# Kernel tuning notes

Measured on AMD Instinct MI355X. Metric: run time of the kernel, lower is better.

The kernel has to match this reference:

```python
import jax, jax.numpy as jnp
import numpy as np

N = 16000
E = 512000
HID = 128
OUT = 64
BN_EPS = 1e-5


def setup_inputs() -> dict:
    key = jax.random.key(0)
    ks = jax.random.split(key, 8)
    x = jax.random.normal(ks[0], (N, HID), dtype=jnp.float32)
    src = jax.random.randint(ks[1], (E,), 0, N, dtype=jnp.int32)
    dst = jax.random.randint(ks[2], (E,), 0, N, dtype=jnp.int32)
    s = 1.0 / np.sqrt(HID)
    fc_w = jax.random.uniform(ks[3], (OUT, HID), jnp.float32, -s, s)
    fc_b = jnp.zeros((OUT,), jnp.float32)
    w1 = jax.random.uniform(ks[4], (HID, HID), jnp.float32, -s, s)
    b1 = jnp.zeros((HID,), jnp.float32)
    w2 = jax.random.uniform(ks[5], (OUT, HID), jnp.float32, -s, s)
    b2 = jnp.zeros((OUT,), jnp.float32)
    epsilon = jnp.full((N,), 0.5, jnp.float32)
    gamma = jnp.ones((OUT,), jnp.float32)
    beta = jnp.zeros((OUT,), jnp.float32)
    return {"x": x, "src": src, "dst": dst, "fc_w": fc_w, "fc_b": fc_b,
            "w1": w1, "b1": b1, "w2": w2, "b2": b2,
            "epsilon": epsilon, "gamma": gamma, "beta": beta}


def _agg(feat, src, dst, n):
    # DGL update_all(copy_src, sum): gather source features, scatter-sum to dst.
    return jax.ops.segment_sum(feat[src], dst, num_segments=n)


def reference(x, src, dst, fc_w, fc_b, w1, b1, w2, b2, epsilon, gamma, beta):
    n = x.shape[0]
    # skip-path linear projection
    h1 = x @ fc_w.T + fc_b                       # [N, OUT]
    # GraphConv layer 1: aggregate then linear, then ReLU
    h2 = jax.nn.relu(_agg(x, src, dst, n) @ w1.T + b1)   # [N, HID]
    # GraphConv layer 2
    h2 = _agg(h2, src, dst, n) @ w2.T + b2       # [N, OUT]
    # per-node epsilon blend
    eps = epsilon[:, None]
    h = (1.0 - eps) * h1 + eps * h2              # [N, OUT]
    # averaged gram matrices
    ret = (h @ h.T + x @ x.T) * 0.5              # [N, N]
    # BatchNorm1d (training mode: biased batch stats)
    mean = jnp.mean(h, axis=0)
    var = jnp.mean(jnp.square(h - mean), axis=0)
    hn = (h - mean) * jax.lax.rsqrt(var + BN_EPS) * gamma + beta
    return ret, hn
```

## Files before the change

kernel.cpp:

```cpp
#include <hip/hip_runtime.h>
#include <hip/hip_bf16.h>

typedef __bf16 bf16x8 __attribute__((ext_vector_type(8)));
typedef float  f32x4  __attribute__((ext_vector_type(4)));
typedef unsigned short u16x8 __attribute__((ext_vector_type(8)));

#define HID 128
#define OUT 64
#define BN_EPS 1e-5f

__device__ __forceinline__ float bf2f(unsigned short u) {
  union { unsigned int i; float f; } c; c.i = ((unsigned)u) << 16; return c.f;
}

__global__ __launch_bounds__(256) void xconv_k(
    const float* __restrict__ x, unsigned short* __restrict__ xbf,
    int* __restrict__ cnt, int n)
{
  int gid = blockIdx.x * blockDim.x + threadIdx.x;
  if (gid < n) cnt[gid] = 0;
  int stride = gridDim.x * blockDim.x;
  int total = n * 32;
  for (int idx = gid; idx < total; idx += stride) {
    f32x4 v = ((const f32x4*)x)[idx];
    ushort4 o;
    __bf16 b0 = (__bf16)v[0], b1 = (__bf16)v[1], b2 = (__bf16)v[2], b3 = (__bf16)v[3];
    o.x = *(unsigned short*)&b0; o.y = *(unsigned short*)&b1;
    o.z = *(unsigned short*)&b2; o.w = *(unsigned short*)&b3;
    ((ushort4*)xbf)[idx] = o;
  }
}

__global__ __launch_bounds__(256) void hist_k(
    const int* __restrict__ dst, int* __restrict__ cnt, int e)
{
  int stride = gridDim.x * blockDim.x;
  for (int i = blockIdx.x * blockDim.x + threadIdx.x; i < e; i += stride)
    atomicAdd(&cnt[dst[i]], 1);
}

__global__ __launch_bounds__(256) void scan_k(
    const int* __restrict__ cnt, int* __restrict__ offsets,
    int* __restrict__ cursor, float* __restrict__ stats, int n)
{
  int t = threadIdx.x;
  if (t < 128) stats[t] = 0.f;
  __shared__ int part[256];
  int chunk = (n + 255) / 256;
  int base = t * chunk;
  int s = 0;
  for (int i = 0; i < chunk; ++i) {
    int idx = base + i;
    if (idx < n) s += cnt[idx];
  }
  part[t] = s;
  __syncthreads();
  for (int off = 1; off < 256; off <<= 1) {
    int v = 0;
    if (t >= off) v = part[t - off];
    __syncthreads();
    if (t >= off) part[t] += v;
    __syncthreads();
  }
  int run = (t == 0) ? 0 : part[t - 1];
  for (int i = 0; i < chunk; ++i) {
    int idx = base + i;
    if (idx < n) {
      offsets[idx] = run;
      cursor[idx]  = run;
      run += cnt[idx];
    }
  }
  if (t == 255) offsets[n] = run;
}

__global__ __launch_bounds__(256) void place_k(
    const int* __restrict__ src, const int* __restrict__ dst,
    int* __restrict__ cursor, int* __restrict__ sorted_src, int e)
{
  int stride = gridDim.x * blockDim.x;
  for (int i = blockIdx.x * blockDim.x + threadIdx.x; i < e; i += stride) {
    int pos = atomicAdd(&cursor[dst[i]], 1);
    sorted_src[pos] = src[i];
  }
}

__global__ __launch_bounds__(256) void aggx_k(
    const unsigned short* __restrict__ xbf, const int* __restrict__ sorted_src,
    const int* __restrict__ offsets, float* __restrict__ agg, int n)
{
  int wave = (blockIdx.x * 256 + threadIdx.x) >> 6;
  int lane = threadIdx.x & 63;
  if (wave >= n) return;
  int qtr = lane >> 4;
  int l16 = lane & 15;
  int beg = offsets[wave], end = offsets[wave + 1];
  float a0[8] = {}, a1[8] = {};
  int i = beg + qtr;
  for (; i + 4 < end; i += 8) {
    int s0 = sorted_src[i];
    int s1 = sorted_src[i + 4];
    u16x8 v0 = *(const u16x8*)(xbf + (size_t)s0 * HID + l16 * 8);
    u16x8 v1 = *(const u16x8*)(xbf + (size_t)s1 * HID + l16 * 8);
    #pragma unroll
    for (int j = 0; j < 8; ++j) { a0[j] += bf2f(v0[j]); a1[j] += bf2f(v1[j]); }
  }
  if (i < end) {
    int s0 = sorted_src[i];
    u16x8 v0 = *(const u16x8*)(xbf + (size_t)s0 * HID + l16 * 8);
    #pragma unroll
    for (int j = 0; j < 8; ++j) a0[j] += bf2f(v0[j]);
  }
  #pragma unroll
  for (int j = 0; j < 8; ++j) a0[j] += a1[j];
  #pragma unroll
  for (int j = 0; j < 8; ++j) a0[j] += __shfl_xor(a0[j], 16, 64);
  #pragma unroll
  for (int j = 0; j < 8; ++j) a0[j] += __shfl_xor(a0[j], 32, 64);
  if (qtr == 0) {
    f32x4 lo = {a0[0], a0[1], a0[2], a0[3]};
    f32x4 hi = {a0[4], a0[5], a0[6], a0[7]};
    *(f32x4*)(agg + (size_t)wave * HID + l16 * 8)     = lo;
    *(f32x4*)(agg + (size_t)wave * HID + l16 * 8 + 4) = hi;
  }
}

__global__ __launch_bounds__(256) void agg2y_k(
    const unsigned short* __restrict__ y2, const int* __restrict__ sorted_src,
    const int* __restrict__ offsets, float* __restrict__ aggy, int n)
{
  int wave = (blockIdx.x * 256 + threadIdx.x) >> 6;
  int lane = threadIdx.x & 63;
  if (wave >= n) return;
  int qtr = lane >> 4;
  int l16 = lane & 15;
  int beg = offsets[wave], end = offsets[wave + 1];
  f32x4 a0 = {0.f, 0.f, 0.f, 0.f}, a1 = {0.f, 0.f, 0.f, 0.f};
  int i = beg + qtr;
  for (; i + 4 < end; i += 8) {
    int s0 = sorted_src[i];
    int s1 = sorted_src[i + 4];
    ushort4 v0 = *(const ushort4*)(y2 + (size_t)s0 * OUT + l16 * 4);
    ushort4 v1 = *(const ushort4*)(y2 + (size_t)s1 * OUT + l16 * 4);
    a0[0] += bf2f(v0.x); a0[1] += bf2f(v0.y); a0[2] += bf2f(v0.z); a0[3] += bf2f(v0.w);
    a1[0] += bf2f(v1.x); a1[1] += bf2f(v1.y); a1[2] += bf2f(v1.z); a1[3] += bf2f(v1.w);
  }
  if (i < end) {
    int s0 = sorted_src[i];
    ushort4 v0 = *(const ushort4*)(y2 + (size_t)s0 * OUT + l16 * 4);
    a0[0] += bf2f(v0.x); a0[1] += bf2f(v0.y); a0[2] += bf2f(v0.z); a0[3] += bf2f(v0.w);
  }
  a0 += a1;
  f32x4 other;
  #pragma unroll
  for (int j = 0; j < 4; ++j) other[j] = __shfl_xor(a0[j], 16, 64);
  a0 += other;
  #pragma unroll
  for (int j = 0; j < 4; ++j) other[j] = __shfl_xor(a0[j], 32, 64);
  a0 += other;
  if (qtr == 0)
    *(f32x4*)(aggy + (size_t)wave * OUT + l16 * 4) = a0;
}

__global__ __launch_bounds__(256) void mlp_fused_k(
    const float* __restrict__ agg, const float* __restrict__ w1,
    const float* __restrict__ b1, const float* __restrict__ w2,
    unsigned short* __restrict__ y2, int n)
{
  __shared__ float aggs[16][132];
  __shared__ float h2s[16][132];
  int t = threadIdx.x;
  int rbase = blockIdx.x * 16;

  for (int idx = t; idx < 16 * 32; idx += 256) {
    int r = idx >> 5, c = idx & 31;
    ((f32x4*)&aggs[r][0])[c] = ((const f32x4*)(agg + (size_t)(rbase + r) * HID))[c];
  }
  __syncthreads();

  {
    int j = t & 127, rh = t >> 7;
    const f32x4* w1r = (const f32x4*)(w1 + (size_t)j * HID);
    float acc[8];
    float bj = b1[j];
    #pragma unroll
    for (int p = 0; p < 8; ++p) acc[p] = bj;
    for (int k = 0; k < 32; ++k) {
      f32x4 w = w1r[k];
      #pragma unroll
      for (int p = 0; p < 8; ++p) {
        f32x4 a = ((const f32x4*)&aggs[rh * 8 + p][0])[k];
        acc[p] += w[0] * a[0] + w[1] * a[1] + w[2] * a[2] + w[3] * a[3];
      }
    }
    #pragma unroll
    for (int p = 0; p < 8; ++p) h2s[rh * 8 + p][j] = fmaxf(acc[p], 0.f);
  }
  __syncthreads();

  {
    int o = t & 63, rq = t >> 6;
    const f32x4* w2r = (const f32x4*)(w2 + (size_t)o * HID);
    float acc[4] = {0.f, 0.f, 0.f, 0.f};
    for (int k = 0; k < 32; ++k) {
      f32x4 w = w2r[k];
      #pragma unroll
      for (int p = 0; p < 4; ++p) {
        f32x4 a = ((const f32x4*)&h2s[rq + p * 4][0])[k];
        acc[p] += w[0] * a[0] + w[1] * a[1] + w[2] * a[2] + w[3] * a[3];
      }
    }
    #pragma unroll
    for (int p = 0; p < 4; ++p) {
      __bf16 b = (__bf16)acc[p];
      y2[(size_t)(rbase + rq + p * 4) * OUT + o] = *(unsigned short*)&b;
    }
  }
}

__global__ __launch_bounds__(256) void combine_k(
    const float* __restrict__ x, const float* __restrict__ aggy,
    const float* __restrict__ fcw, const float* __restrict__ fcb,
    const float* __restrict__ b2,
    const float* __restrict__ eps, float* __restrict__ h,
    unsigned short* __restrict__ hbf, float* __restrict__ stats, int n)
{
  __shared__ float xs[32][132];
  __shared__ float ls[256], lss[256];
  int t = threadIdx.x;
  int rbase = blockIdx.x * 32;

  for (int idx = t; idx < 32 * 32; idx += 256) {
    int r = idx >> 5, c = idx & 31;
    ((f32x4*)&xs[r][0])[c] = ((const f32x4*)(x + (size_t)(rbase + r) * HID))[c];
  }
  __syncthreads();

  int o = t & 63, rq = t >> 6;
  const f32x4* fwr = (const f32x4*)(fcw + (size_t)o * HID);
  float fb = fcb[o], bb = b2[o];
  float acc[8];
  #pragma unroll
  for (int p = 0; p < 8; ++p) acc[p] = fb;
  for (int k = 0; k < 32; ++k) {
    f32x4 w = fwr[k];
    #pragma unroll
    for (int p = 0; p < 8; ++p) {
      f32x4 a = ((const f32x4*)&xs[rq + p * 4][0])[k];
      acc[p] += w[0] * a[0] + w[1] * a[1] + w[2] * a[2] + w[3] * a[3];
    }
  }
  float s = 0.f, ss = 0.f;
  #pragma unroll
  for (int p = 0; p < 8; ++p) {
    int row = rbase + rq + p * 4;
    float a2 = aggy[(size_t)row * OUT + o] + bb;
    float ev = eps[row];
    float hv = (1.f - ev) * acc[p] + ev * a2;
    h[(size_t)row * OUT + o] = hv;
    __bf16 hb = (__bf16)hv;
    hbf[(size_t)row * OUT + o] = *(unsigned short*)&hb;
    s += hv; ss += hv * hv;
  }
  ls[t] = s; lss[t] = ss;
  __syncthreads();
  if (t < 64) {
    s  = ls[t]  + ls[t + 64]  + ls[t + 128]  + ls[t + 192];
    ss = lss[t] + lss[t + 64] + lss[t + 128] + lss[t + 192];
    atomicAdd(&stats[t], s);
    atomicAdd(&stats[64 + t], ss);
  }
}

__global__ __launch_bounds__(256) void hn_k(
    const float* __restrict__ h, const float* __restrict__ stats,
    const float* __restrict__ gamma, const float* __restrict__ beta,
    float* __restrict__ outp, int n)
{
  int stride = gridDim.x * blockDim.x;
  int total  = n * OUT;
  float inv_n = 1.f / (float)n;
  for (int idx = blockIdx.x * blockDim.x + threadIdx.x; idx < total; idx += stride) {
    int col = idx & 63;
    float mean = stats[col] * inv_n;
    float var  = stats[64 + col] * inv_n - mean * mean;
    float sc   = rsqrtf(var + BN_EPS) * gamma[col];
    outp[idx] = (h[idx] - mean) * sc + beta[col];
  }
}

__global__ __launch_bounds__(256, 3) void gemm_k(
    const unsigned short* __restrict__ hbf, const unsigned short* __restrict__ xbf,
    float* __restrict__ out, int n, int nwg)
{
  __shared__ char pool[64 * 132 * 4];
  __bf16* As = (__bf16*)pool;
  __bf16* Bs = (__bf16*)(pool + 16384);
  float*  T  = (float*)pool;

  int nb = n >> 7;
  int orig = blockIdx.x;
  int q = nwg >> 3, r = nwg & 7;
  int xcd = orig & 7, idx8 = orig >> 3;
  int bid = (xcd < r ? xcd * (q + 1) : r * (q + 1) + (xcd - r) * q) + idx8;

  int bi = 0, rem = bid;
  while (rem >= nb - bi) { rem -= nb - bi; ++bi; }
  int bj = bi + rem;
  int t = threadIdx.x;
  int w = t >> 6, lane = t & 63;
  int wr = (w >> 1) << 6;
  int wc = (w & 1) << 6;
  int lr = lane & 15, lg = lane >> 4;

  const uint4* ha = (const uint4*)(hbf + (size_t)bi * 128 * OUT);
  const uint4* hb = (const uint4*)(hbf + (size_t)bj * 128 * OUT);
  const uint4* xa = (const uint4*)(xbf + (size_t)bi * 128 * HID);
  const uint4* xb = (const uint4*)(xbf + (size_t)bj * 128 * HID);
  uint4* Asv = (uint4*)As;
  uint4* Bsv = (uint4*)Bs;

  f32x4 acc[4][4] = {};
  #pragma unroll
  for (int kc = 0; kc < 3; ++kc) {
    #pragma unroll
    for (int it = 0; it < 4; ++it) {
      int ch = t + it * 256;
      int row = ch >> 3, c = ch & 7;
      int sw = row * 8 + (c ^ (row & 7));
      uint4 va, vb;
      if (kc == 0) { va = ha[row * 8 + c];                  vb = hb[row * 8 + c]; }
      else         { va = xa[row * 16 + (kc - 1) * 8 + c];  vb = xb[row * 16 + (kc - 1) * 8 + c]; }
      Asv[sw] = va;
      Bsv[sw] = vb;
    }
    __syncthreads();
    const bf16x8* Ac = (const bf16x8*)As;
    const bf16x8* Bc = (const bf16x8*)Bs;
    #pragma unroll
    for (int ks = 0; ks < 2; ++ks) {
      bf16x8 a[4], b[4];
      #pragma unroll
      for (int m = 0; m < 4; ++m) {
        int ar = wr + m * 16 + lr;
        int br = wc + m * 16 + lr;
        a[m] = Ac[ar * 8 + ((ks * 4 + lg) ^ (ar & 7))];
        b[m] = Bc[br * 8 + ((ks * 4 + lg) ^ (br & 7))];
      }
      #pragma unroll
      for (int m = 0; m < 4; ++m)
        #pragma unroll
        for (int nn = 0; nn < 4; ++nn)
          acc[m][nn] = __builtin_amdgcn_mfma_f32_16x16x32_bf16(a[m], b[nn], acc[m][nn], 0, 0, 0);
    }
    __syncthreads();
  }

  #pragma unroll
  for (int m = 0; m < 4; ++m)
    #pragma unroll
    for (int nn = 0; nn < 4; ++nn)
      acc[m][nn] = acc[m][nn] * 0.5f;

  size_t N = (size_t)n;

  if (bi != bj) {
    #pragma unroll
    for (int p = 0; p < 2; ++p) {
      if ((wc >> 6) == p) {
        #pragma unroll
        for (int m = 0; m < 4; ++m)
          #pragma unroll
          for (int nn = 0; nn < 4; ++nn) {
            int c  = nn * 16 + lr;
            int r0 = wr + m * 16 + lg * 4;
            *(f32x4*)&T[c * 132 + r0] = acc[m][nn];
          }
      }
      __syncthreads();
      #pragma unroll
      for (int it = 0; it < 8; ++it) {
        int idx = t + it * 256;
        int rr = idx >> 5, c4 = idx & 31;
        f32x4 v = *(const f32x4*)&T[rr * 132 + c4 * 4];
        *(f32x4*)&out[(size_t)(bj * 128 + p * 64 + rr) * N + bi * 128 + c4 * 4] = v;
      }
      __syncthreads();
    }
  }

  #pragma unroll
  for (int m = 0; m < 4; ++m) {
    size_t gr0 = (size_t)(bi * 128 + wr + m * 16 + lg * 4);
    #pragma unroll
    for (int nn = 0; nn < 4; ++nn) {
      int gc = bj * 128 + wc + nn * 16 + lr;
      #pragma unroll
      for (int r = 0; r < 4; ++r)
        out[(gr0 + r) * N + gc] = acc[m][nn][r];
    }
  }
}

extern "C" void kernel_launch(void* const* d_in, const int* in_sizes, int n_in,
                              void* d_out, int out_size, void* d_ws, size_t ws_size,
                              hipStream_t stream) {
  const float* x    = (const float*)d_in[0];
  const int*   src  = (const int*)d_in[1];
  const int*   dst  = (const int*)d_in[2];
  const float* fcw  = (const float*)d_in[3];
  const float* fcb  = (const float*)d_in[4];
  const float* w1   = (const float*)d_in[5];
  const float* b1   = (const float*)d_in[6];
  const float* w2   = (const float*)d_in[7];
  const float* b2   = (const float*)d_in[8];
  const float* eps  = (const float*)d_in[9];
  const float* gamma= (const float*)d_in[10];
  const float* beta = (const float*)d_in[11];
  int n = in_sizes[0] / HID;
  int e = in_sizes[1];
  float* out = (float*)d_out;

  char* ws = (char*)d_ws;
  size_t off = 0;
  float* agg   = (float*)(ws + off); off += (size_t)n * HID * 4;
  float* h     = (float*)(ws + off); off += (size_t)n * OUT * 4;
  float* aggy  = (float*)(ws + off); off += (size_t)n * OUT * 4;
  unsigned short* xbf = (unsigned short*)(ws + off); off += (size_t)n * HID * 2;
  unsigned short* hbf = (unsigned short*)(ws + off); off += (size_t)n * OUT * 2;
  unsigned short* y2  = (unsigned short*)(ws + off); off += (size_t)n * OUT * 2;
  float* stats = (float*)(ws + off); off += 512;
  int* cnt     = (int*)(ws + off); off += (size_t)n * 4;
  int* offsets = (int*)(ws + off); off += (size_t)(n + 1) * 4;
  int* cursor  = (int*)(ws + off); off += (size_t)n * 4;
  int* sorted_src = (int*)(ws + off); off += (size_t)e * 4;

  xconv_k<<<2048, 256, 0, stream>>>(x, xbf, cnt, n);
  hist_k<<<512, 256, 0, stream>>>(dst, cnt, e);
  scan_k<<<1, 256, 0, stream>>>(cnt, offsets, cursor, stats, n);
  place_k<<<512, 256, 0, stream>>>(src, dst, cursor, sorted_src, e);

  aggx_k<<<(n * 64 + 255) / 256, 256, 0, stream>>>(xbf, sorted_src, offsets, agg, n);
  mlp_fused_k<<<n / 16, 256, 0, stream>>>(agg, w1, b1, w2, y2, n);
  agg2y_k<<<(n * 64 + 255) / 256, 256, 0, stream>>>(y2, sorted_src, offsets, aggy, n);
  combine_k<<<n / 32, 256, 0, stream>>>(x, aggy, fcw, fcb, b2, eps, h, hbf, stats, n);
  hn_k<<<1024, 256, 0, stream>>>(h, stats, gamma, beta, out + (size_t)n * n, n);

  int nb = n >> 7;
  int nwg = nb * (nb + 1) / 2;
  gemm_k<<<nwg, 256, 0, stream>>>(hbf, xbf, out, n, nwg);
}
```

Measured before the change: 398.6 us.

## Fuse neighbor aggregation into MLP and combine kernels, shrink CSR indices

Moves both gather-sum aggregations into the consumer kernels (mlp_fused_k and combine_k), which write the aggregated rows to shared memory instead of round-tripping fp32 agg and aggy buffers through global memory. It also merges the x conversion and degree histogram into one prep kernel with a memset for counts. The scan is widened to 1024 threads, and source indices are stored as 16-bit values. Risks: fewer waves per node in the fused kernels may reduce gather parallelism, and the 16-bit indices only hold when N fits in 65536.

```diff
diff --git a/kernel.cpp b/kernel.cpp
--- a/kernel.cpp
+++ b/kernel.cpp
@@ -13,12 +13,11 @@
   union { unsigned int i; float f; } c; c.i = ((unsigned)u) << 16; return c.f;
 }
 
-__global__ __launch_bounds__(256) void xconv_k(
+__global__ __launch_bounds__(256) void prep_k(
     const float* __restrict__ x, unsigned short* __restrict__ xbf,
-    int* __restrict__ cnt, int n)
+    const int* __restrict__ dst, int* __restrict__ cnt, int n, int e)
 {
   int gid = blockIdx.x * blockDim.x + threadIdx.x;
-  if (gid < n) cnt[gid] = 0;
   int stride = gridDim.x * blockDim.x;
   int total = n * 32;
   for (int idx = gid; idx < total; idx += stride) {
@@ -29,24 +28,18 @@
     o.z = *(unsigned short*)&b2; o.w = *(unsigned short*)&b3;
     ((ushort4*)xbf)[idx] = o;
   }
-}
-
-__global__ __launch_bounds__(256) void hist_k(
-    const int* __restrict__ dst, int* __restrict__ cnt, int e)
-{
-  int stride = gridDim.x * blockDim.x;
-  for (int i = blockIdx.x * blockDim.x + threadIdx.x; i < e; i += stride)
+  for (int i = gid; i < e; i += stride)
     atomicAdd(&cnt[dst[i]], 1);
 }
 
-__global__ __launch_bounds__(256) void scan_k(
+__global__ __launch_bounds__(1024) void scan_k(
     const int* __restrict__ cnt, int* __restrict__ offsets,
     int* __restrict__ cursor, float* __restrict__ stats, int n)
 {
   int t = threadIdx.x;
   if (t < 128) stats[t] = 0.f;
-  __shared__ int part[256];
-  int chunk = (n + 255) / 256;
+  __shared__ int part[1024];
+  int chunk = (n + 1023) / 1024;
   int base = t * chunk;
   int s = 0;
   for (int i = 0; i < chunk; ++i) {
@@ -55,7 +48,7 @@
   }
   part[t] = s;
   __syncthreads();
-  for (int off = 1; off < 256; off <<= 1) {
+  for (int off = 1; off < 1024; off <<= 1) {
     int v = 0;
     if (t >= off) v = part[t - off];
     __syncthreads();
@@ -71,110 +64,65 @@
       run += cnt[idx];
     }
   }
-  if (t == 255) offsets[n] = run;
+  if (t == 1023) offsets[n] = run;
 }
 
 __global__ __launch_bounds__(256) void place_k(
     const int* __restrict__ src, const int* __restrict__ dst,
-    int* __restrict__ cursor, int* __restrict__ sorted_src, int e)
+    int* __restrict__ cursor, unsigned short* __restrict__ sorted_src, int e)
 {
   int stride = gridDim.x * blockDim.x;
   for (int i = blockIdx.x * blockDim.x + threadIdx.x; i < e; i += stride) {
     int pos = atomicAdd(&cursor[dst[i]], 1);
-    sorted_src[pos] = src[i];
-  }
-}
-
-__global__ __launch_bounds__(256) void aggx_k(
-    const unsigned short* __restrict__ xbf, const int* __restrict__ sorted_src,
-    const int* __restrict__ offsets, float* __restrict__ agg, int n)
-{
-  int wave = (blockIdx.x * 256 + threadIdx.x) >> 6;
-  int lane = threadIdx.x & 63;
-  if (wave >= n) return;
-  int qtr = lane >> 4;
-  int l16 = lane & 15;
-  int beg = offsets[wave], end = offsets[wave + 1];
-  float a0[8] = {}, a1[8] = {};
-  int i = beg + qtr;
-  for (; i + 4 < end; i += 8) {
-    int s0 = sorted_src[i];
-    int s1 = sorted_src[i + 4];
-    u16x8 v0 = *(const u16x8*)(xbf + (size_t)s0 * HID + l16 * 8);
-    u16x8 v1 = *(const u16x8*)(xbf + (size_t)s1 * HID + l16 * 8);
-    #pragma unroll
-    for (int j = 0; j < 8; ++j) { a0[j] += bf2f(v0[j]); a1[j] += bf2f(v1[j]); }
-  }
-  if (i < end) {
-    int s0 = sorted_src[i];
-    u16x8 v0 = *(const u16x8*)(xbf + (size_t)s0 * HID + l16 * 8);
-    #pragma unroll
-    for (int j = 0; j < 8; ++j) a0[j] += bf2f(v0[j]);
-  }
-  #pragma unroll
-  for (int j = 0; j < 8; ++j) a0[j] += a1[j];
-  #pragma unroll
-  for (int j = 0; j < 8; ++j) a0[j] += __shfl_xor(a0[j], 16, 64);
-  #pragma unroll
-  for (int j = 0; j < 8; ++j) a0[j] += __shfl_xor(a0[j], 32, 64);
-  if (qtr == 0) {
-    f32x4 lo = {a0[0], a0[1], a0[2], a0[3]};
-    f32x4 hi = {a0[4], a0[5], a0[6], a0[7]};
-    *(f32x4*)(agg + (size_t)wave * HID + l16 * 8)     = lo;
-    *(f32x4*)(agg + (size_t)wave * HID + l16 * 8 + 4) = hi;
-  }
-}
-
-__global__ __launch_bounds__(256) void agg2y_k(
-    const unsigned short* __restrict__ y2, const int* __restrict__ sorted_src,
-    const int* __restrict__ offsets, float* __restrict__ aggy, int n)
-{
-  int wave = (blockIdx.x * 256 + threadIdx.x) >> 6;
-  int lane = threadIdx.x & 63;
-  if (wave >= n) return;
-  int qtr = lane >> 4;
-  int l16 = lane & 15;
-  int beg = offsets[wave], end = offsets[wave + 1];
-  f32x4 a0 = {0.f, 0.f, 0.f, 0.f}, a1 = {0.f, 0.f, 0.f, 0.f};
-  int i = beg + qtr;
-  for (; i + 4 < end; i += 8) {
-    int s0 = sorted_src[i];
-    int s1 = sorted_src[i + 4];
-    ushort4 v0 = *(const ushort4*)(y2 + (size_t)s0 * OUT + l16 * 4);
-    ushort4 v1 = *(const ushort4*)(y2 + (size_t)s1 * OUT + l16 * 4);
-    a0[0] += bf2f(v0.x); a0[1] += bf2f(v0.y); a0[2] += bf2f(v0.z); a0[3] += bf2f(v0.w);
-    a1[0] += bf2f(v1.x); a1[1] += bf2f(v1.y); a1[2] += bf2f(v1.z); a1[3] += bf2f(v1.w);
-  }
-  if (i < end) {
-    int s0 = sorted_src[i];
-    ushort4 v0 = *(const ushort4*)(y2 + (size_t)s0 * OUT + l16 * 4);
-    a0[0] += bf2f(v0.x); a0[1] += bf2f(v0.y); a0[2] += bf2f(v0.z); a0[3] += bf2f(v0.w);
-  }
-  a0 += a1;
-  f32x4 other;
-  #pragma unroll
-  for (int j = 0; j < 4; ++j) other[j] = __shfl_xor(a0[j], 16, 64);
-  a0 += other;
-  #pragma unroll
-  for (int j = 0; j < 4; ++j) other[j] = __shfl_xor(a0[j], 32, 64);
-  a0 += other;
-  if (qtr == 0)
-    *(f32x4*)(aggy + (size_t)wave * OUT + l16 * 4) = a0;
+    sorted_src[pos] = (unsigned short)src[i];
+  }
 }
 
 __global__ __launch_bounds__(256) void mlp_fused_k(
-    const float* __restrict__ agg, const float* __restrict__ w1,
-    const float* __restrict__ b1, const float* __restrict__ w2,
-    unsigned short* __restrict__ y2, int n)
+    const unsigned short* __restrict__ xbf, const unsigned short* __restrict__ sorted_src,
+    const int* __restrict__ offsets,
+    const float* __restrict__ w1, const float* __restrict__ b1,
+    const float* __restrict__ w2, unsigned short* __restrict__ y2, int n)
 {
   __shared__ float aggs[16][132];
   __shared__ float h2s[16][132];
   int t = threadIdx.x;
   int rbase = blockIdx.x * 16;
-
-  for (int idx = t; idx < 16 * 32; idx += 256) {
-    int r = idx >> 5, c = idx & 31;
-    ((f32x4*)&aggs[r][0])[c] = ((const f32x4*)(agg + (size_t)(rbase + r) * HID))[c];
+  int wave = t >> 6, lane = t & 63;
+  int qtr = lane >> 4, l16 = lane & 15;
+
+  for (int nd = 0; nd < 4; ++nd) {
+    int r = wave * 4 + nd;
+    int node = rbase + r;
+    int beg = offsets[node], end = offsets[node + 1];
+    float a0[8] = {}, a1[8] = {};
+    int i = beg + qtr;
+    for (; i + 4 < end; i += 8) {
+      int s0 = sorted_src[i];
+      int s1 = sorted_src[i + 4];
+      u16x8 v0 = *(const u16x8*)(xbf + (size_t)s0 * HID + l16 * 8);
+      u16x8 v1 = *(const u16x8*)(xbf + (size_t)s1 * HID + l16 * 8);
+      #pragma unroll
+      for (int j = 0; j < 8; ++j) { a0[j] += bf2f(v0[j]); a1[j] += bf2f(v1[j]); }
+    }
+    if (i < end) {
+      int s0 = sorted_src[i];
+      u16x8 v0 = *(const u16x8*)(xbf + (size_t)s0 * HID + l16 * 8);
+      #pragma unroll
+      for (int j = 0; j < 8; ++j) a0[j] += bf2f(v0[j]);
+    }
+    #pragma unroll
+    for (int j = 0; j < 8; ++j) a0[j] += a1[j];
+    #pragma unroll
+    for (int j = 0; j < 8; ++j) a0[j] += __shfl_xor(a0[j], 16, 64);
+    #pragma unroll
+    for (int j = 0; j < 8; ++j) a0[j] += __shfl_xor(a0[j], 32, 64);
+    if (qtr == 0) {
+      f32x4 lo = {a0[0], a0[1], a0[2], a0[3]};
+      f32x4 hi = {a0[4], a0[5], a0[6], a0[7]};
+      *(f32x4*)&aggs[r][l16 * 8]     = lo;
+      *(f32x4*)&aggs[r][l16 * 8 + 4] = hi;
+    }
   }
   __syncthreads();
 
@@ -219,20 +167,55 @@
 }
 
 __global__ __launch_bounds__(256) void combine_k(
-    const float* __restrict__ x, const float* __restrict__ aggy,
+    const float* __restrict__ x, const unsigned short* __restrict__ y2,
+    const unsigned short* __restrict__ sorted_src, const int* __restrict__ offsets,
     const float* __restrict__ fcw, const float* __restrict__ fcb,
     const float* __restrict__ b2,
     const float* __restrict__ eps, float* __restrict__ h,
     unsigned short* __restrict__ hbf, float* __restrict__ stats, int n)
 {
   __shared__ float xs[32][132];
+  __shared__ float ay[32][68];
   __shared__ float ls[256], lss[256];
   int t = threadIdx.x;
   int rbase = blockIdx.x * 32;
+  int wave = t >> 6, lane = t & 63;
+  int qtr = lane >> 4, l16 = lane & 15;
 
   for (int idx = t; idx < 32 * 32; idx += 256) {
     int r = idx >> 5, c = idx & 31;
     ((f32x4*)&xs[r][0])[c] = ((const f32x4*)(x + (size_t)(rbase + r) * HID))[c];
+  }
+
+  for (int nd = 0; nd < 8; ++nd) {
+    int r = wave * 8 + nd;
+    int node = rbase + r;
+    int beg = offsets[node], end = offsets[node + 1];
+    f32x4 a0 = {0.f, 0.f, 0.f, 0.f}, a1 = {0.f, 0.f, 0.f, 0.f};
+    int i = beg + qtr;
+    for (; i + 4 < end; i += 8) {
+      int s0 = sorted_src[i];
+      int s1 = sorted_src[i + 4];
+      ushort4 v0 = *(const ushort4*)(y2 + (size_t)s0 * OUT + l16 * 4);
+      ushort4 v1 = *(const ushort4*)(y2 + (size_t)s1 * OUT + l16 * 4);
+      a0[0] += bf2f(v0.x); a0[1] += bf2f(v0.y); a0[2] += bf2f(v0.z); a0[3] += bf2f(v0.w);
+      a1[0] += bf2f(v1.x); a1[1] += bf2f(v1.y); a1[2] += bf2f(v1.z); a1[3] += bf2f(v1.w);
+    }
+    if (i < end) {
+      int s0 = sorted_src[i];
+      ushort4 v0 = *(const ushort4*)(y2 + (size_t)s0 * OUT + l16 * 4);
+      a0[0] += bf2f(v0.x); a0[1] += bf2f(v0.y); a0[2] += bf2f(v0.z); a0[3] += bf2f(v0.w);
+    }
+    a0 += a1;
+    f32x4 other;
+    #pragma unroll
+    for (int j = 0; j < 4; ++j) other[j] = __shfl_xor(a0[j], 16, 64);
+    a0 += other;
+    #pragma unroll
+    for (int j = 0; j < 4; ++j) other[j] = __shfl_xor(a0[j], 32, 64);
+    a0 += other;
+    if (qtr == 0)
+      *(f32x4*)&ay[r][l16 * 4] = a0;
   }
   __syncthreads();
 
@@ -253,8 +236,9 @@
   float s = 0.f, ss = 0.f;
   #pragma unroll
   for (int p = 0; p < 8; ++p) {
-    int row = rbase + rq + p * 4;
-    float a2 = aggy[(size_t)row * OUT + o] + bb;
+    int rl = rq + p * 4;
+    int row = rbase + rl;
+    float a2 = ay[rl][o] + bb;
     float ev = eps[row];
     float hv = (1.f - ev) * acc[p] + ev * a2;
     h[(size_t)row * OUT + o] = hv;
@@ -423,9 +407,7 @@
 
   char* ws = (char*)d_ws;
   size_t off = 0;
-  float* agg   = (float*)(ws + off); off += (size_t)n * HID * 4;
   float* h     = (float*)(ws + off); off += (size_t)n * OUT * 4;
-  float* aggy  = (float*)(ws + off); off += (size_t)n * OUT * 4;
   unsigned short* xbf = (unsigned short*)(ws + off); off += (size_t)n * HID * 2;
   unsigned short* hbf = (unsigned short*)(ws + off); off += (size_t)n * OUT * 2;
   unsigned short* y2  = (unsigned short*)(ws + off); off += (size_t)n * OUT * 2;
@@ -433,17 +415,17 @@
   int* cnt     = (int*)(ws + off); off += (size_t)n * 4;
   int* offsets = (int*)(ws + off); off += (size_t)(n + 1) * 4;
   int* cursor  = (int*)(ws + off); off += (size_t)n * 4;
-  int* sorted_src = (int*)(ws + off); off += (size_t)e * 4;
-
-  xconv_k<<<2048, 256, 0, stream>>>(x, xbf, cnt, n);
-  hist_k<<<512, 256, 0, stream>>>(dst, cnt, e);
-  scan_k<<<1, 256, 0, stream>>>(cnt, offsets, cursor, stats, n);
+  unsigned short* sorted_src = (unsigned short*)(ws + off); off += (size_t)e * 2;
+
+  hipMemsetAsync(cnt, 0, (size_t)n * 4, stream);
+
+  prep_k<<<2048, 256, 0, stream>>>(x, xbf, dst, cnt, n, e);
+  scan_k<<<1, 1024, 0, stream>>>(cnt, offsets, cursor, stats, n);
   place_k<<<512, 256, 0, stream>>>(src, dst, cursor, sorted_src, e);
 
-  aggx_k<<<(n * 64 + 255) / 256, 256, 0, stream>>>(xbf, sorted_src, offsets, agg, n);
-  mlp_fused_k<<<n / 16, 256, 0, stream>>>(agg, w1, b1, w2, y2, n);
-  agg2y_k<<<(n * 64 + 255) / 256, 256, 0, stream>>>(y2, sorted_src, offsets, aggy, n);
-  combine_k<<<n / 32, 256, 0, stream>>>(x, aggy, fcw, fcb, b2, eps, h, hbf, stats, n);
+  mlp_fused_k<<<n / 16, 256, 0, stream>>>(xbf, sorted_src, offsets, w1, b1, w2, y2, n);
+  combine_k<<<n / 32, 256, 0, stream>>>(x, y2, sorted_src, offsets, fcw, fcb, b2, eps,
+                                        h, hbf, stats, n);
   hn_k<<<1024, 256, 0, stream>>>(h, stats, gamma, beta, out + (size_t)n * n, n);
 
   int nb = n >> 7;
```

Result: slower. 413.7 us (+3.8%).
